# Kernel optimization log

Measured on AMD Instinct MI355X. Metric: run time of the kernel, lower is better.

Reference implementation:

```python
import jax, jax.numpy as jnp
import numpy as np

K = 16          # filter order (number of Laplacian powers)
MLP_OUT = 16    # mlp_hid == mlp_out for mlp_nlayers == 1
D_PE = 64       # phi output dim
BN_EPS = 1e-5
B, N, M = 8, 1024, 128
E = 131072


def setup_inputs() -> dict:
    key = jax.random.key(0)
    ks = jax.random.split(key, 12)
    # Symmetric, spectrally-bounded Laplacian surrogate so 15 matrix powers stay finite.
    A = jax.random.normal(ks[0], (B, N, N), dtype=jnp.float32)
    Lap = (A + jnp.swapaxes(A, -1, -2)) * (0.5 / jnp.sqrt(jnp.float32(N)))
    W = jax.random.normal(ks[1], (B, N, M), dtype=jnp.float32)
    edge_index = jax.random.randint(ks[2], (2, E), 0, B * N, dtype=jnp.int64)
    batch = jnp.repeat(jnp.arange(B, dtype=jnp.int64), N)
    # MLP layer (k -> MLP_OUT) + BatchNorm affine params
    lin_w = jax.random.normal(ks[3], (K, MLP_OUT), dtype=jnp.float32) / jnp.sqrt(jnp.float32(K))
    lin_b = jnp.zeros((MLP_OUT,), dtype=jnp.float32)
    bn_gamma = jnp.ones((MLP_OUT,), dtype=jnp.float32)
    bn_beta = jnp.zeros((MLP_OUT,), dtype=jnp.float32)
    # phi: GIN-style 2-layer MLP after neighbor aggregation
    phi_w1 = jax.random.normal(ks[4], (MLP_OUT, D_PE), dtype=jnp.float32) / jnp.sqrt(jnp.float32(MLP_OUT))
    phi_b1 = jnp.zeros((D_PE,), dtype=jnp.float32)
    phi_w2 = jax.random.normal(ks[5], (D_PE, D_PE), dtype=jnp.float32) / jnp.sqrt(jnp.float32(D_PE))
    phi_b2 = jnp.zeros((D_PE,), dtype=jnp.float32)
    return {"Lap": Lap, "W": W, "lin_w": lin_w, "lin_b": lin_b,
            "bn_gamma": bn_gamma, "bn_beta": bn_beta,
            "phi_w1": phi_w1, "phi_b1": phi_b1, "phi_w2": phi_w2, "phi_b2": phi_b2,
            "edge_index": edge_index, "batch": batch}


def _filter(S, W0):
    """Sequential power filter: returns [k, N, M] = [W0, S@W0, S^2@W0, ...]."""
    def step(out, _):
        nxt = S @ out
        return nxt, nxt
    _, rest = jax.lax.scan(step, W0, None, length=K - 1)
    return jnp.concatenate([W0[None], rest], axis=0)


def reference(Lap, W, lin_w, lin_b, bn_gamma, bn_beta,
              phi_w1, phi_b1, phi_w2, phi_b2, edge_index, batch):
    # Batched filter over all graphs: [B, k, N, M] -> [B, N, M, k]
    feat = jax.vmap(_filter)(Lap, W)
    feat = jnp.transpose(feat, (0, 2, 3, 1))
    # Linear over k -> MLP_OUT channels: [B, N, M, C]
    h = feat @ lin_w + lin_b
    # BatchNorm1d (training mode), per-graph statistics over (N, M) per channel,
    # matching the torch per-graph loop where BN sees [M, C, N].
    mean = jnp.mean(h, axis=(1, 2), keepdims=True)
    var = jnp.var(h, axis=(1, 2), keepdims=True)
    h = (h - mean) * jax.lax.rsqrt(var + BN_EPS) * bn_gamma + bn_beta
    h = jax.nn.relu(h)
    # phi: pool random-sample dim M, flatten graphs -> [N_sum, C]
    x = jnp.mean(h, axis=2).reshape(-1, h.shape[-1])
    src, dst = edge_index[0], edge_index[1]
    agg = jax.ops.segment_sum(x[src], dst, num_segments=x.shape[0])
    g = x + agg  # GIN aggregation
    out = jax.nn.relu(g @ phi_w1 + phi_b1) @ phi_w2 + phi_b2  # [N_sum, D_PE]
    return out
```

## Files before the change

kernel.cpp:

```cpp
#include <hip/hip_runtime.h>

#define B 8
#define N 1024
#define M 128
#define KF 16
#define C 16
#define DPE 64
#define NE 131072
#define NV (B*N)
#define NM (N*M)
#define BN_EPS 1e-5f

typedef short bf16x8 __attribute__((ext_vector_type(8)));
typedef float f32x4 __attribute__((ext_vector_type(4)));

__device__ inline unsigned short f2bf_rne(float f) {
    unsigned u = __float_as_uint(f);
    u += 0x7fffu + ((u >> 16) & 1u);
    return (unsigned short)(u >> 16);
}
__device__ inline void split_bf16(float v, unsigned short& hi, unsigned short& lo) {
    hi = f2bf_rne(v);
    float hf = __uint_as_float((unsigned)hi << 16);
    lo = f2bf_rne(v - hf);
}
union U4 { uint4 v; unsigned short s[8]; };

__device__ __host__ inline size_t SF4(int b, int nsub, int ks, int hl, int l) {
    return ((((size_t)b * 64 + nsub) * 32 + ks) * 2 + hl) * 64 + l;
}
__device__ __host__ inline size_t PF4(int b, int msub, int ks, int hl, int l) {
    return ((((size_t)b * 8 + msub) * 32 + ks) * 2 + hl) * 64 + l;
}
#define PFBUF ((size_t)B * 8 * 32 * 2 * 64)

__global__ __launch_bounds__(256) void prep_s(const float* __restrict__ Lap, uint4* __restrict__ Sf) {
    int b = blockIdx.x & 7, nb = blockIdx.x >> 3;
    int t = threadIdx.x;
    int nl = t >> 4, kg = t & 15;
    int n = nb * 16 + nl;
    const float* row = Lap + ((size_t)b * N + n) * N;
    #pragma unroll
    for (int jj = 0; jj < 8; jj++) {
        int koct = kg + 16 * jj;
        int k0 = koct * 8;
        float4 f0 = *(const float4*)(row + k0);
        float4 f1 = *(const float4*)(row + k0 + 4);
        float e[8] = {f0.x, f0.y, f0.z, f0.w, f1.x, f1.y, f1.z, f1.w};
        U4 hi, lo;
        #pragma unroll
        for (int j = 0; j < 8; j++) split_bf16(e[j], hi.s[j], lo.s[j]);
        int ks = k0 >> 5;
        int lf = nl + 16 * (koct & 3);
        Sf[SF4(b, nb, ks, 0, lf)] = hi.v;
        Sf[SF4(b, nb, ks, 1, lf)] = lo.v;
    }
}

__global__ __launch_bounds__(256) void prep_w_plane(const float* __restrict__ W, float* __restrict__ feat) {
    __shared__ float T[32][33];
    int b = blockIdx.x & 7;
    int tile = blockIdx.x >> 3;
    int nt = tile & 31, mt = tile >> 5;
    int n0 = nt * 32, m0 = mt * 32;
    int t = threadIdx.x;
    {
        int nl = t >> 3, mq = t & 7;
        float4 v = *(const float4*)(W + ((size_t)b * N + n0 + nl) * M + m0 + mq * 4);
        T[nl][mq * 4 + 0] = v.x; T[nl][mq * 4 + 1] = v.y;
        T[nl][mq * 4 + 2] = v.z; T[nl][mq * 4 + 3] = v.w;
    }
    __syncthreads();
    {
        int ml = t >> 3, nq = t & 7;
        float4 v = make_float4(T[nq * 4 + 0][ml], T[nq * 4 + 1][ml], T[nq * 4 + 2][ml], T[nq * 4 + 3][ml]);
        float* plane = feat + (size_t)b * KF * NM;
        *(float4*)(plane + (size_t)(m0 + ml) * N + n0 + nq * 4) = v;
    }
}

__global__ __launch_bounds__(256) void prep_w_frag(const float* __restrict__ W, uint4* __restrict__ Pf) {
    int b = blockIdx.x & 7;
    int r = (blockIdx.x >> 3) * 256 + threadIdx.x;
    int msub = r >> 11, ks = (r >> 6) & 31, l = r & 63;
    int m = 16 * msub + (l & 15);
    U4 hi, lo;
    #pragma unroll
    for (int j = 0; j < 8; j++) {
        int n = 32 * ks + 8 * (l >> 4) + j;
        float v = W[((size_t)b * N + n) * M + m];
        split_bf16(v, hi.s[j], lo.s[j]);
    }
    Pf[PF4(b, msub, ks, 0, l)] = hi.v;
    Pf[PF4(b, msub, ks, 1, l)] = lo.v;
}

__global__ __launch_bounds__(512) void gemm_chain(const uint4* __restrict__ Sf,
                                                  uint4* __restrict__ PfA,
                                                  uint4* __restrict__ PfB,
                                                  float* __restrict__ feat,
                                                  unsigned* bar) {
    extern __shared__ __align__(16) char smem[];
    uint4* ldsS = (uint4*)smem;
    float* Dl = (float*)(smem + 131072);

    int b = blockIdx.x & 7, bx = blockIdx.x >> 3;
    int t = threadIdx.x;
    int w = t >> 6, lane = t & 63;
    size_t sbase = SF4(b, 2 * bx, 0, 0, 0);
    int n0 = 32 * bx;

    #pragma unroll
    for (int i = 0; i < 16; i++) ldsS[t + 512 * i] = Sf[sbase + t + 512 * i];
    __syncthreads();

    #pragma unroll 1
    for (int k = 0; k < KF - 1; k++) {
        const uint4* PfIn = (k & 1) ? PfB : PfA;
        uint4* PfOut      = (k & 1) ? PfA : PfB;
        const uint4* Pw = PfIn + (size_t)(b * 8 + w) * 4096;

        f32x4 acc0 = {}, acc1 = {};
        uint4 ph[4], pl[4];
        #pragma unroll
        for (int q = 0; q < 4; q++) {
            ph[q] = Pw[(size_t)q * 128 + lane];
            pl[q] = Pw[(size_t)q * 128 + 64 + lane];
        }
        #pragma unroll 4
        for (int ks = 0; ks < 32; ks++) {
            uint4 ahu = ph[ks & 3], alu = pl[ks & 3];
            if (ks < 28) {
                ph[ks & 3] = Pw[(size_t)(ks + 4) * 128 + lane];
                pl[ks & 3] = Pw[(size_t)(ks + 4) * 128 + 64 + lane];
            }
            bf16x8 b0h = __builtin_bit_cast(bf16x8, ldsS[ks * 128 + lane]);
            bf16x8 b0l = __builtin_bit_cast(bf16x8, ldsS[ks * 128 + 64 + lane]);
            bf16x8 b1h = __builtin_bit_cast(bf16x8, ldsS[4096 + ks * 128 + lane]);
            bf16x8 b1l = __builtin_bit_cast(bf16x8, ldsS[4096 + ks * 128 + 64 + lane]);
            bf16x8 Ah = __builtin_bit_cast(bf16x8, ahu);
            bf16x8 Al = __builtin_bit_cast(bf16x8, alu);
            acc0 = __builtin_amdgcn_mfma_f32_16x16x32_bf16(Ah, b0h, acc0, 0, 0, 0);
            acc0 = __builtin_amdgcn_mfma_f32_16x16x32_bf16(Ah, b0l, acc0, 0, 0, 0);
            acc0 = __builtin_amdgcn_mfma_f32_16x16x32_bf16(Al, b0h, acc0, 0, 0, 0);
            acc1 = __builtin_amdgcn_mfma_f32_16x16x32_bf16(Ah, b1h, acc1, 0, 0, 0);
            acc1 = __builtin_amdgcn_mfma_f32_16x16x32_bf16(Ah, b1l, acc1, 0, 0, 0);
            acc1 = __builtin_amdgcn_mfma_f32_16x16x32_bf16(Al, b1h, acc1, 0, 0, 0);
        }

        #pragma unroll
        for (int r = 0; r < 4; r++) {
            int m = 16 * w + 4 * (lane >> 4) + r;
            Dl[m * 36 + (lane & 15)] = acc0[r];
            Dl[m * 36 + 16 + (lane & 15)] = acc1[r];
        }
        __syncthreads();
        {
            int m = t >> 2, c0 = (t & 3) * 8;
            float* plane = feat + ((size_t)b * KF + (k + 1)) * NM + (size_t)m * N + n0 + c0;
            ((float4*)plane)[0] = *(const float4*)&Dl[m * 36 + c0];
            ((float4*)plane)[1] = *(const float4*)&Dl[m * 36 + c0 + 4];
        }
        if (k < KF - 2) {
            {
                int l = t & 63;
                int m = 16 * w + (l & 15);
                int ncol = 8 * (l >> 4);
                float4 v0 = *(const float4*)&Dl[m * 36 + ncol];
                float4 v1 = *(const float4*)&Dl[m * 36 + ncol + 4];
                float e[8] = {v0.x, v0.y, v0.z, v0.w, v1.x, v1.y, v1.z, v1.w};
                U4 hi, lo;
                #pragma unroll
                for (int j = 0; j < 8; j++) split_bf16(e[j], hi.s[j], lo.s[j]);
                PfOut[PF4(b, w, bx, 0, l)] = hi.v;
                PfOut[PF4(b, w, bx, 1, l)] = lo.v;
            }
            __syncthreads();
            if (t == 0) {
                __hip_atomic_fetch_add(&bar[b * 32], 1u, __ATOMIC_RELAXED,
                                       __HIP_MEMORY_SCOPE_AGENT);
                unsigned target = 32u * (unsigned)(k + 1);
                while (__hip_atomic_load(&bar[b * 32], __ATOMIC_RELAXED,
                                         __HIP_MEMORY_SCOPE_AGENT) < target)
                    __builtin_amdgcn_s_sleep(1);
            }
            __syncthreads();
            asm volatile("buffer_inv sc0\n\ts_waitcnt vmcnt(0)" ::: "memory");
        } else {
            __syncthreads();
        }
    }
}

__global__ __launch_bounds__(256) void bn_stats(const float* __restrict__ feat,
                                                const float* __restrict__ lin_w,
                                                const float* __restrict__ lin_b,
                                                float* __restrict__ stats) {
    __shared__ float wls[KF * C];
    __shared__ float red[4][2][C];
    int t = threadIdx.x;
    wls[t] = lin_w[t];
    __syncthreads();
    int b = blockIdx.x & 7;
    int i = (blockIdx.x >> 3) * 256 + t;
    const float4* fb = (const float4*)(feat + (size_t)b * KF * NM);

    float4 hacc[C];
    #pragma unroll
    for (int c = 0; c < C; c++) {
        float bb = lin_b[c];
        hacc[c] = make_float4(bb, bb, bb, bb);
    }
    for (int kk = 0; kk < KF; kk++) {
        float4 pv = fb[(size_t)kk * (NM / 4) + i];
        #pragma unroll
        for (int c = 0; c < C; c++) {
            float wv = wls[kk * C + c];
            hacc[c].x = fmaf(pv.x, wv, hacc[c].x);
            hacc[c].y = fmaf(pv.y, wv, hacc[c].y);
            hacc[c].z = fmaf(pv.z, wv, hacc[c].z);
            hacc[c].w = fmaf(pv.w, wv, hacc[c].w);
        }
    }
    float s[C], ss[C];
    #pragma unroll
    for (int c = 0; c < C; c++) {
        float4 h = hacc[c];
        s[c] = h.x + h.y + h.z + h.w;
        ss[c] = h.x * h.x + h.y * h.y + h.z * h.z + h.w * h.w;
    }
    #pragma unroll
    for (int off = 32; off > 0; off >>= 1)
        #pragma unroll
        for (int c = 0; c < C; c++) {
            s[c] += __shfl_down(s[c], off);
            ss[c] += __shfl_down(ss[c], off);
        }
    if ((t & 63) == 0) {
        int wv = t >> 6;
        #pragma unroll
        for (int c = 0; c < C; c++) { red[wv][0][c] = s[c]; red[wv][1][c] = ss[c]; }
    }
    __syncthreads();
    if (t < 32) {
        int which = t >> 4, c = t & 15;
        float v = red[0][which][c] + red[1][which][c] + red[2][which][c] + red[3][which][c];
        atomicAdd(&stats[b * 32 + which * 16 + c], v);
    }
}

__global__ __launch_bounds__(256) void bn_x(const float* __restrict__ feat,
                                            const float* __restrict__ lin_w,
                                            const float* __restrict__ lin_b,
                                            const float* __restrict__ gam,
                                            const float* __restrict__ bet,
                                            const float* __restrict__ stats,
                                            float* __restrict__ x) {
    __shared__ float wls[KF * C];
    __shared__ float red[8][32 * 17];
    int t = threadIdx.x;
    wls[t] = lin_w[t];
    __syncthreads();
    int grp = blockIdx.x;
    int b = grp & 7, n0 = (grp >> 3) * 32;
    int nl = t & 31, mg = t >> 5;
    int n = n0 + nl;

    const float inv_nm = 1.0f / (float)NM;
    float sc[C], sh[C], bb[C];
    #pragma unroll
    for (int c = 0; c < C; c++) {
        float mean = stats[b * 32 + c] * inv_nm;
        float var = stats[b * 32 + 16 + c] * inv_nm - mean * mean;
        sc[c] = gam[c] * rsqrtf(var + BN_EPS);
        sh[c] = bet[c] - mean * sc[c];
        bb[c] = lin_b[c];
    }
    const float* fb = feat + (size_t)b * KF * NM + n;
    float y[C] = {};
    for (int m = mg * 16; m < mg * 16 + 16; m++) {
        float p[KF];
        #pragma unroll
        for (int kk = 0; kk < KF; kk++) p[kk] = fb[(size_t)kk * NM + (size_t)m * N];
        #pragma unroll
        for (int c = 0; c < C; c++) {
            float h = bb[c];
            #pragma unroll
            for (int kk = 0; kk < KF; kk++) h = fmaf(p[kk], wls[kk * C + c], h);
            y[c] += fmaxf(fmaf(h, sc[c], sh[c]), 0.0f);
        }
    }
    #pragma unroll
    for (int c = 0; c < C; c++) red[mg][nl * 17 + c] = y[c];
    __syncthreads();
    #pragma unroll
    for (int q = 0; q < 2; q++) {
        int slot = t + q * 256;
        int snl = slot >> 4, c = slot & 15;
        float v = 0.0f;
        #pragma unroll
        for (int m8 = 0; m8 < 8; m8++) v += red[m8][snl * 17 + c];
        v *= (1.0f / (float)M);
        x[((size_t)b * N + n0 + snl) * C + c] = v;
    }
}

__global__ __launch_bounds__(256) void edge_hist(const int* __restrict__ ei, int* __restrict__ cnt) {
    int e = blockIdx.x * 256 + threadIdx.x;
    bool is64 = (ei[1] == 0 && ei[3] == 0 && ei[5] == 0 && ei[7] == 0);
    int dst = is64 ? ei[2 * (NE + e)] : ei[NE + e];
    atomicAdd(&cnt[dst], 1);
}

__global__ __launch_bounds__(256) void edge_scan(const int* __restrict__ cnt,
                                                 int* __restrict__ off, int* __restrict__ cur) {
    __shared__ int ss[256];
    int t = threadIdx.x;
    int base = t * 32;
    int local[32];
    int s = 0;
    #pragma unroll
    for (int i = 0; i < 32; i++) { local[i] = cnt[base + i]; s += local[i]; }
    ss[t] = s;
    __syncthreads();
    #pragma unroll
    for (int d = 1; d < 256; d <<= 1) {
        int v = (t >= d) ? ss[t - d] : 0;
        __syncthreads();
        ss[t] += v;
        __syncthreads();
    }
    int excl = ss[t] - s;
    #pragma unroll
    for (int i = 0; i < 32; i++) { off[base + i] = excl; cur[base + i] = excl; excl += local[i]; }
}

__global__ __launch_bounds__(256) void edge_fill(const int* __restrict__ ei,
                                                 int* __restrict__ cur, int* __restrict__ bucket) {
    int e = blockIdx.x * 256 + threadIdx.x;
    bool is64 = (ei[1] == 0 && ei[3] == 0 && ei[5] == 0 && ei[7] == 0);
    int src, dst;
    if (is64) { src = ei[2 * e]; dst = ei[2 * (NE + e)]; }
    else      { src = ei[e];     dst = ei[NE + e]; }
    int pos = atomicAdd(&cur[dst], 1);
    bucket[pos] = src;
}

__global__ __launch_bounds__(256) void phi_fused(const int* __restrict__ cnt,
                                                 const int* __restrict__ off,
                                                 const int* __restrict__ bucket,
                                                 const float* __restrict__ x,
                                                 const float* __restrict__ w1,
                                                 const float* __restrict__ b1,
                                                 const float* __restrict__ w2,
                                                 const float* __restrict__ b2,
                                                 float* __restrict__ out) {
    __shared__ float w1s[C * DPE];
    __shared__ float w2s[DPE * DPE];
    __shared__ float b2s[DPE];
    __shared__ float gsh[16][17];
    __shared__ float h1sh[16][DPE];
    int t = threadIdx.x;
    #pragma unroll
    for (int q = 0; q < 4; q++) w1s[t + q * 256] = w1[t + q * 256];
    #pragma unroll
    for (int q = 0; q < 16; q++) w2s[t + q * 256] = w2[t + q * 256];
    if (t < DPE) b2s[t] = b2[t];

    {
        int nl = t >> 4, c = t & 15;
        int n = blockIdx.x * 16 + nl;
        int o = off[n], d = cnt[n];
        float v = x[(size_t)n * C + c];
        int j = 0;
        for (; j + 4 <= d; j += 4) {
            int s0 = bucket[o + j], s1 = bucket[o + j + 1];
            int s2 = bucket[o + j + 2], s3 = bucket[o + j + 3];
            v += x[(size_t)s0 * C + c];
            v += x[(size_t)s1 * C + c];
            v += x[(size_t)s2 * C + c];
            v += x[(size_t)s3 * C + c];
        }
        for (; j < d; j++) v += x[(size_t)bucket[o + j] * C + c];
        gsh[nl][c] = v;
    }
    __syncthreads();
    #pragma unroll
    for (int q = 0; q < 4; q++) {
        int item = t + 256 * q;
        int node = item >> 6, j = item & 63;
        float h = b1[j];
        #pragma unroll
        for (int c = 0; c < C; c++) h = fmaf(gsh[node][c], w1s[c * DPE + j], h);
        h1sh[node][j] = fmaxf(h, 0.0f);
    }
    __syncthreads();
    #pragma unroll
    for (int q = 0; q < 4; q++) {
        int item = t + 256 * q;
        int node = item >> 6, d = item & 63;
        float o2 = b2s[d];
        #pragma unroll
        for (int j = 0; j < DPE; j++) o2 = fmaf(h1sh[node][j], w2s[j * DPE + d], o2);
        out[((size_t)blockIdx.x * 16 + node) * DPE + d] = o2;
    }
}

extern "C" void kernel_launch(void* const* d_in, const int* in_sizes, int n_in,
                              void* d_out, int out_size, void* d_ws, size_t ws_size,
                              hipStream_t stream) {
    const float* Lap   = (const float*)d_in[0];
    const float* W     = (const float*)d_in[1];
    const float* lin_w = (const float*)d_in[2];
    const float* lin_b = (const float*)d_in[3];
    const float* gam   = (const float*)d_in[4];
    const float* bet   = (const float*)d_in[5];
    const float* w1    = (const float*)d_in[6];
    const float* b1    = (const float*)d_in[7];
    const float* w2    = (const float*)d_in[8];
    const float* b2    = (const float*)d_in[9];
    const int*   ei    = (const int*)d_in[10];

    char* wsb = (char*)d_ws;
    float* feat  = (float*)wsb;
    uint4* Sf    = (uint4*)(wsb + ((size_t)64 << 20));
    uint4* Pf    = (uint4*)(wsb + ((size_t)96 << 20));
    float* stats = (float*)(wsb + ((size_t)104 << 20));
    unsigned* bar = (unsigned*)(stats + 256);
    float* x     = stats + 2048;
    int*   cnt   = (int*)(x + (size_t)NV * C);
    int*   off   = cnt + NV;
    int*   cur   = off + NV;
    int*   bucket= cur + NV;
    float* out   = (float*)d_out;

    static bool attr_set = false;
    if (!attr_set) {
        hipFuncSetAttribute((const void*)gemm_chain,
                            hipFuncAttributeMaxDynamicSharedMemorySize, 149504);
        attr_set = true;
    }

    hipMemsetAsync(stats, 0, 8192, stream);
    hipMemsetAsync(cnt, 0, NV * sizeof(int), stream);
    prep_s<<<dim3(512), 256, 0, stream>>>(Lap, Sf);
    prep_w_plane<<<dim3(1024), 256, 0, stream>>>(W, feat);
    prep_w_frag<<<dim3(512), 256, 0, stream>>>(W, Pf);
    gemm_chain<<<dim3(256), 512, 149504, stream>>>(Sf, Pf, Pf + PFBUF, feat, bar);
    bn_stats<<<dim3(1024), 256, 0, stream>>>(feat, lin_w, lin_b, stats);
    bn_x<<<dim3(256), 256, 0, stream>>>(feat, lin_w, lin_b, gam, bet, stats, x);
    edge_hist<<<dim3(NE / 256), 256, 0, stream>>>(ei, cnt);
    edge_scan<<<dim3(1), 256, 0, stream>>>(cnt, off, cur);
    edge_fill<<<dim3(NE / 256), 256, 0, stream>>>(ei, cur, bucket);
    phi_fused<<<dim3(NV / 16), 256, 0, stream>>>(cnt, off, bucket, x, w1, b1, w2, b2, out);
}
```

Measured before the change: 317.7 us.

## Split GEMM chain K dimension across wave groups with 2x2 register tiles

```diff
diff --git a/kernel.cpp b/kernel.cpp
--- a/kernel.cpp
+++ b/kernel.cpp
@@ -107,6 +107,7 @@
     int b = blockIdx.x & 7, bx = blockIdx.x >> 3;
     int t = threadIdx.x;
     int w = t >> 6, lane = t & 63;
+    int g = w >> 2, wq = w & 3;
     size_t sbase = SF4(b, 2 * bx, 0, 0, 0);
     int n0 = 32 * bx;
 
@@ -118,41 +119,75 @@
     for (int k = 0; k < KF - 1; k++) {
         const uint4* PfIn = (k & 1) ? PfB : PfA;
         uint4* PfOut      = (k & 1) ? PfA : PfB;
-        const uint4* Pw = PfIn + (size_t)(b * 8 + w) * 4096;
-
-        f32x4 acc0 = {}, acc1 = {};
-        uint4 ph[4], pl[4];
-        #pragma unroll
-        for (int q = 0; q < 4; q++) {
-            ph[q] = Pw[(size_t)q * 128 + lane];
-            pl[q] = Pw[(size_t)q * 128 + 64 + lane];
-        }
-        #pragma unroll 4
-        for (int ks = 0; ks < 32; ks++) {
-            uint4 ahu = ph[ks & 3], alu = pl[ks & 3];
-            if (ks < 28) {
-                ph[ks & 3] = Pw[(size_t)(ks + 4) * 128 + lane];
-                pl[ks & 3] = Pw[(size_t)(ks + 4) * 128 + 64 + lane];
+        const uint4* Pw0 = PfIn + (size_t)(b * 8 + 2 * wq) * 4096 + (size_t)(16 * g) * 128;
+        const uint4* Pw1 = Pw0 + 4096;
+
+        f32x4 acc[2][2] = {};
+        uint4 ph[2][2], pl[2][2];
+        #pragma unroll
+        for (int q = 0; q < 2; q++) {
+            ph[q][0] = Pw0[(size_t)q * 128 + lane];
+            pl[q][0] = Pw0[(size_t)q * 128 + 64 + lane];
+            ph[q][1] = Pw1[(size_t)q * 128 + lane];
+            pl[q][1] = Pw1[(size_t)q * 128 + 64 + lane];
+        }
+        #pragma unroll 2
+        for (int ks = 0; ks < 16; ks++) {
+            int kg = 16 * g + ks;
+            uint4 a0h = ph[ks & 1][0], a0l = pl[ks & 1][0];
+            uint4 a1h = ph[ks & 1][1], a1l = pl[ks & 1][1];
+            if (ks < 14) {
+                ph[ks & 1][0] = Pw0[(size_t)(ks + 2) * 128 + lane];
+                pl[ks & 1][0] = Pw0[(size_t)(ks + 2) * 128 + 64 + lane];
+                ph[ks & 1][1] = Pw1[(size_t)(ks + 2) * 128 + lane];
+                pl[ks & 1][1] = Pw1[(size_t)(ks + 2) * 128 + 64 + lane];
             }
-            bf16x8 b0h = __builtin_bit_cast(bf16x8, ldsS[ks * 128 + lane]);
-            bf16x8 b0l = __builtin_bit_cast(bf16x8, ldsS[ks * 128 + 64 + lane]);
-            bf16x8 b1h = __builtin_bit_cast(bf16x8, ldsS[4096 + ks * 128 + lane]);
-            bf16x8 b1l = __builtin_bit_cast(bf16x8, ldsS[4096 + ks * 128 + 64 + lane]);
-            bf16x8 Ah = __builtin_bit_cast(bf16x8, ahu);
-            bf16x8 Al = __builtin_bit_cast(bf16x8, alu);
-            acc0 = __builtin_amdgcn_mfma_f32_16x16x32_bf16(Ah, b0h, acc0, 0, 0, 0);
-            acc0 = __builtin_amdgcn_mfma_f32_16x16x32_bf16(Ah, b0l, acc0, 0, 0, 0);
-            acc0 = __builtin_amdgcn_mfma_f32_16x16x32_bf16(Al, b0h, acc0, 0, 0, 0);
-            acc1 = __builtin_amdgcn_mfma_f32_16x16x32_bf16(Ah, b1h, acc1, 0, 0, 0);
-            acc1 = __builtin_amdgcn_mfma_f32_16x16x32_bf16(Ah, b1l, acc1, 0, 0, 0);
-            acc1 = __builtin_amdgcn_mfma_f32_16x16x32_bf16(Al, b1h, acc1, 0, 0, 0);
-        }
-
-        #pragma unroll
-        for (int r = 0; r < 4; r++) {
-            int m = 16 * w + 4 * (lane >> 4) + r;
-            Dl[m * 36 + (lane & 15)] = acc0[r];
-            Dl[m * 36 + 16 + (lane & 15)] = acc1[r];
+            bf16x8 b0h = __builtin_bit_cast(bf16x8, ldsS[kg * 128 + lane]);
+            bf16x8 b0l = __builtin_bit_cast(bf16x8, ldsS[kg * 128 + 64 + lane]);
+            bf16x8 b1h = __builtin_bit_cast(bf16x8, ldsS[4096 + kg * 128 + lane]);
+            bf16x8 b1l = __builtin_bit_cast(bf16x8, ldsS[4096 + kg * 128 + 64 + lane]);
+            bf16x8 A0h = __builtin_bit_cast(bf16x8, a0h);
+            bf16x8 A0l = __builtin_bit_cast(bf16x8, a0l);
+            bf16x8 A1h = __builtin_bit_cast(bf16x8, a1h);
+            bf16x8 A1l = __builtin_bit_cast(bf16x8, a1l);
+            acc[0][0] = __builtin_amdgcn_mfma_f32_16x16x32_bf16(A0h, b0h, acc[0][0], 0, 0, 0);
+            acc[0][0] = __builtin_amdgcn_mfma_f32_16x16x32_bf16(A0h, b0l, acc[0][0], 0, 0, 0);
+            acc[0][0] = __builtin_amdgcn_mfma_f32_16x16x32_bf16(A0l, b0h, acc[0][0], 0, 0, 0);
+            acc[0][1] = __builtin_amdgcn_mfma_f32_16x16x32_bf16(A0h, b1h, acc[0][1], 0, 0, 0);
+            acc[0][1] = __builtin_amdgcn_mfma_f32_16x16x32_bf16(A0h, b1l, acc[0][1], 0, 0, 0);
+            acc[0][1] = __builtin_amdgcn_mfma_f32_16x16x32_bf16(A0l, b1h, acc[0][1], 0, 0, 0);
+            acc[1][0] = __builtin_amdgcn_mfma_f32_16x16x32_bf16(A1h, b0h, acc[1][0], 0, 0, 0);
+            acc[1][0] = __builtin_amdgcn_mfma_f32_16x16x32_bf16(A1h, b0l, acc[1][0], 0, 0, 0);
+            acc[1][0] = __builtin_amdgcn_mfma_f32_16x16x32_bf16(A1l, b0h, acc[1][0], 0, 0, 0);
+            acc[1][1] = __builtin_amdgcn_mfma_f32_16x16x32_bf16(A1h, b1h, acc[1][1], 0, 0, 0);
+            acc[1][1] = __builtin_amdgcn_mfma_f32_16x16x32_bf16(A1h, b1l, acc[1][1], 0, 0, 0);
+            acc[1][1] = __builtin_amdgcn_mfma_f32_16x16x32_bf16(A1l, b1h, acc[1][1], 0, 0, 0);
+        }
+
+        if (g == 1) {
+            #pragma unroll
+            for (int mi = 0; mi < 2; mi++)
+                #pragma unroll
+                for (int ni = 0; ni < 2; ni++)
+                    #pragma unroll
+                    for (int r = 0; r < 4; r++) {
+                        int m = 32 * wq + 16 * mi + 4 * (lane >> 4) + r;
+                        int c = 16 * ni + (lane & 15);
+                        Dl[m * 36 + c] = acc[mi][ni][r];
+                    }
+        }
+        __syncthreads();
+        if (g == 0) {
+            #pragma unroll
+            for (int mi = 0; mi < 2; mi++)
+                #pragma unroll
+                for (int ni = 0; ni < 2; ni++)
+                    #pragma unroll
+                    for (int r = 0; r < 4; r++) {
+                        int m = 32 * wq + 16 * mi + 4 * (lane >> 4) + r;
+                        int c = 16 * ni + (lane & 15);
+                        Dl[m * 36 + c] += acc[mi][ni][r];
+                    }
         }
         __syncthreads();
         {
```

Result: no change. 313.7 us (-1.3%).
